# Performance work log

Hardware: AMD Instinct MI355X
Metric: run time of the kernel (lower is better)

Reference implementation:

```python
import jax, jax.numpy as jnp
import numpy as np

# Jamba mamba mixer dims
H = 4096      # hidden_size
D = 8192      # intermediate_size = mamba_expand * hidden_size
N = 16        # ssm_state_size (mamba_d_state)
K = 4         # conv_kernel_size (mamba_d_conv)
R = 256       # time_step_rank (mamba_dt_rank)
BATCH = 1
L = 2048
EPS = 1e-6


def setup_inputs() -> dict:
    key = jax.random.key(0)
    ks = jax.random.split(key, 10)
    s = 0.02
    return {
        "hidden_states": jax.random.normal(ks[0], (BATCH, L, H), jnp.float32),
        "W_in": jax.random.normal(ks[1], (2 * D, H), jnp.float32) * s,
        "conv_w": jax.random.normal(ks[2], (D, K), jnp.float32) * s,
        "conv_b": jax.random.normal(ks[3], (D,), jnp.float32) * s,
        "Wx": jax.random.normal(ks[4], (R + 2 * N, D), jnp.float32) * s,
        "dt_ln_w": jnp.ones((R,), jnp.float32),
        "b_ln_w": jnp.ones((N,), jnp.float32),
        "c_ln_w": jnp.ones((N,), jnp.float32),
        "Wdt": jax.random.normal(ks[5], (D, R), jnp.float32) * s,
        "dt_bias": jax.random.normal(ks[6], (D,), jnp.float32) * s,
        "A": -jnp.exp(jax.random.normal(ks[7], (D, N), jnp.float32) * 0.5),  # A = -exp(A_log)
        "D_param": jnp.ones((D,), jnp.float32),
        "W_out": jax.random.normal(ks[8], (H, D), jnp.float32) * s,
    }


def _rmsnorm(x, w):
    return x * jax.lax.rsqrt(jnp.mean(x * x, axis=-1, keepdims=True) + EPS) * w


def reference(hidden_states, W_in, conv_w, conv_b, Wx, dt_ln_w, b_ln_w, c_ln_w,
              Wdt, dt_bias, A, D_param, W_out):
    # in_proj -> [B, L, 2D]; split into ssm branch and gate
    proj = hidden_states @ W_in.T
    u, gate = jnp.split(proj, 2, axis=-1)

    # causal depthwise conv1d over sequence dim, then SiLU (causal_conv1d_fn)
    x = jnp.transpose(u, (0, 2, 1))  # [B, D, L]
    x = jax.lax.conv_general_dilated(
        x, conv_w[:, None, :], window_strides=(1,), padding=[(K - 1, 0)],
        dimension_numbers=("NCH", "OIH", "NCH"), feature_group_count=D)
    u = jax.nn.silu(jnp.transpose(x, (0, 2, 1)) + conv_b)  # [B, L, D]

    # x_proj -> dt / B / C with RMSNorms
    ssm_p = u @ Wx.T  # [B, L, R + 2N]
    dt, Bm, Cm = jnp.split(ssm_p, [R, R + N], axis=-1)
    dt = _rmsnorm(dt, dt_ln_w)
    Bm = _rmsnorm(Bm, b_ln_w)
    Cm = _rmsnorm(Cm, c_ln_w)

    # dt_proj (skip_bias_add: bias folded into softplus, delta_softplus=True)
    delta = jax.nn.softplus(dt @ Wdt.T + dt_bias)  # [B, L, D]

    # selective scan: state [B, D, N], recurrence over L
    def step(state, xs):
        d_t, B_t, C_t, u_t = xs  # [B,D], [B,N], [B,N], [B,D]
        dA = jnp.exp(d_t[..., None] * A)                       # [B, D, N]
        state = dA * state + (d_t * u_t)[..., None] * B_t[:, None, :]
        y_t = jnp.einsum("bdn,bn->bd", state, C_t)
        return state, y_t

    init = jnp.zeros((hidden_states.shape[0], D, N), hidden_states.dtype)
    xs = (jnp.swapaxes(delta, 0, 1), jnp.swapaxes(Bm, 0, 1),
          jnp.swapaxes(Cm, 0, 1), jnp.swapaxes(u, 0, 1))
    _, ys = jax.lax.scan(step, init, xs)  # ys: [L, B, D]

    y = jnp.swapaxes(ys, 0, 1) + u * D_param   # skip connection u * D
    y = y * jax.nn.silu(gate)                  # gated output
    return y @ W_out.T                         # out_proj -> [B, L, H]
```

## Files before the change

### kernel.cpp

```cpp
#include <hip/hip_runtime.h>
#include <stdint.h>


#define LSEQ 2048
#define HDIM 4096
#define DDIM 8192
#define NST  16
#define NPAD 384
#define NC   16
#define CLEN 128

typedef __bf16 bf16x8 __attribute__((ext_vector_type(8)));
typedef float  f32x4  __attribute__((ext_vector_type(4)));

__device__ __forceinline__ ushort f2b(float f) {
  uint32_t x = __float_as_uint(f);
  x += 0x7FFFu + ((x >> 16) & 1u);
  return (ushort)(x >> 16);
}
__device__ __forceinline__ float b2f(ushort u) {
  return __uint_as_float(((uint32_t)u) << 16);
}

__device__ __forceinline__ void gload_lds16(const ushort* g, ushort* l) {
  __builtin_amdgcn_global_load_lds(
      (const __attribute__((address_space(1))) void*)g,
      (__attribute__((address_space(3))) void*)l, 16, 0, 0);
}

__global__ __launch_bounds__(256) void cvt_kernel(const float* __restrict__ s,
                                                  ushort* __restrict__ d,
                                                  size_t n8) {
  size_t i = (size_t)blockIdx.x * 256 + threadIdx.x;
  if (i >= n8) return;
  const float4* sp = (const float4*)s;
  float4 a = sp[2 * i], b = sp[2 * i + 1];
  union { ushort us[8]; uint4 v; } u;
  u.us[0] = f2b(a.x); u.us[1] = f2b(a.y); u.us[2] = f2b(a.z); u.us[3] = f2b(a.w);
  u.us[4] = f2b(b.x); u.us[5] = f2b(b.y); u.us[6] = f2b(b.z); u.us[7] = f2b(b.w);
  ((uint4*)d)[i] = u.v;
}

template <int MODE, int OUT>
__global__ __launch_bounds__(512, 2) void gemm8p(
    const ushort* __restrict__ A, const ushort* __restrict__ Bw,
    void* __restrict__ Cv, int M, int N, int ldk, int Kc) {
  __shared__ __align__(16) ushort As[2][256 * 64];
  __shared__ __align__(16) ushort Bs[2][256 * 64];
  const int tid  = threadIdx.x;
  const int lane = tid & 63;
  const int w    = tid >> 6;
  const int wr   = w >> 2;
  const int wc   = w & 3;

  const int glob = (blockIdx.z * gridDim.y + blockIdx.y) * gridDim.x + blockIdx.x;
  const int k8 = glob & 7, j = glob >> 3;
  int mt, nt, zz;
  if (MODE == 0) {
    mt = j & 7;
    nt = k8 * (gridDim.x >> 3) + (j >> 3);
    zz = 0;
  } else {
    mt = (k8 & 1) * 4 + (j & 3);
    nt = (k8 >> 1) * 4 + ((j >> 2) & 3);
    zz = j >> 4;
  }
  const int m0 = mt * 256, n0 = nt * 256;
  const int kbeg = zz * Kc;
  const int NT = Kc >> 6;

  const int srck = (lane & 7) ^ ((lane >> 3) & 7);
  const int astripe = w >> 2, awl = w & 3;
  const int arow_st = astripe * 128 + awl * 8 + (lane >> 3);
  const ushort* Abase = A + (size_t)(m0 + arow_st) * ldk + kbeg + srck * 8;
  const int aldsb = (astripe * 128 + awl * 8) * 64;
  const int brow_st = w * 8 + (lane >> 3);
  const ushort* Bbase = Bw + (size_t)(n0 + brow_st) * ldk + kbeg + srck * 8;
  const int bldsb = (w * 8) * 64;

  const int lrow = lane & 15;
  const int kch  = lane >> 4;
  const int axor = lrow & 7;

  auto stA = [&](int buf, int kt, int q) {
    gload_lds16(Abase + (size_t)q * 32 * ldk + kt * 64,
                &As[buf][aldsb + q * 32 * 64]);
  };
  auto stB = [&](int buf, int kt, int half, int jj) {
    gload_lds16(Bbase + (size_t)(half * 128 + jj * 64) * ldk + kt * 64,
                &Bs[buf][bldsb + (half * 128 + jj * 64) * 64]);
  };
  auto rdA = [&](int buf, int mi, int sl) -> bf16x8 {
    int arow = wr * 128 + mi * 16 + lrow;
    int s4 = sl * 4 + kch;
    return *(const bf16x8*)&As[buf][arow * 64 + ((s4 ^ axor) << 3)];
  };
  auto rdB = [&](int buf, int ni, int sl) -> bf16x8 {
    int brow = wc * 64 + ni * 16 + lrow;
    int s4 = sl * 4 + kch;
    return *(const bf16x8*)&Bs[buf][brow * 64 + ((s4 ^ axor) << 3)];
  };

  f32x4 acc[8][4] = {};
  bf16x8 afr[2][2][2];
  bf16x8 bfr[2][4][2];

#define RDAQ(BUF, Q, AP)                                                      \
  { _Pragma("unroll") for (int m2 = 0; m2 < 2; ++m2)                          \
      _Pragma("unroll") for (int sl = 0; sl < 2; ++sl)                        \
        afr[AP][m2][sl] = rdA(BUF, (Q) * 2 + m2, sl); }
#define RDBALL(BUF, BP)                                                       \
  { _Pragma("unroll") for (int ni = 0; ni < 4; ++ni)                          \
      _Pragma("unroll") for (int sl = 0; sl < 2; ++sl)                        \
        bfr[BP][ni][sl] = rdB(BUF, ni, sl); }
#define MFMA16(MQ, AP, BP)                                                    \
  { asm volatile("s_barrier" ::: "memory");                                   \
    __builtin_amdgcn_s_setprio(1);                                            \
    _Pragma("unroll") for (int sl = 0; sl < 2; ++sl)                          \
      _Pragma("unroll") for (int m2 = 0; m2 < 2; ++m2)                        \
        _Pragma("unroll") for (int ni = 0; ni < 4; ++ni)                      \
          acc[(MQ) * 2 + m2][ni] = __builtin_amdgcn_mfma_f32_16x16x32_bf16(   \
              afr[AP][m2][sl], bfr[BP][ni][sl], acc[(MQ) * 2 + m2][ni],       \
              0, 0, 0);                                                       \
    __builtin_amdgcn_s_setprio(0); }

  stB(0, 0, 0, 0); stB(0, 0, 0, 1); stB(0, 0, 1, 0); stB(0, 0, 1, 1);
  stA(0, 0, 0); stA(0, 0, 1); stA(0, 0, 2); stA(0, 0, 3);
  stB(1, 1, 0, 0); stB(1, 1, 0, 1); stB(1, 1, 1, 0); stB(1, 1, 1, 1);
  stA(1, 1, 0); stA(1, 1, 1); stA(1, 1, 2); stA(1, 1, 3);
  asm volatile("s_waitcnt vmcnt(8)" ::: "memory");
  asm volatile("s_barrier" ::: "memory");
  RDBALL(0, 0);
  RDAQ(0, 0, 1);

  for (int t = 0; t < NT; t += 2) {
    const int t2 = (t + 2 < NT) ? t + 2 : 0;
    const int t3 = (t + 3 < NT) ? t + 3 : 0;
    RDAQ(0, 1, 0);
    stB(0, t2, 0, 0); stB(0, t2, 0, 1);
    MFMA16(0, 1, 0);
    RDAQ(0, 2, 1);
    stB(0, t2, 1, 0); stB(0, t2, 1, 1);
    MFMA16(1, 0, 0);
    RDAQ(0, 3, 0);
    stA(0, t2, 0); stA(0, t2, 1);
    MFMA16(2, 1, 0);
    asm volatile("s_waitcnt vmcnt(6)" ::: "memory");
    RDBALL(1, 1);
    RDAQ(1, 0, 1);
    stA(0, t2, 2); stA(0, t2, 3);
    MFMA16(3, 0, 0);
    RDAQ(1, 1, 0);
    stB(1, t3, 0, 0); stB(1, t3, 0, 1);
    MFMA16(0, 1, 1);
    RDAQ(1, 2, 1);
    stB(1, t3, 1, 0); stB(1, t3, 1, 1);
    MFMA16(1, 0, 1);
    RDAQ(1, 3, 0);
    stA(1, t3, 0); stA(1, t3, 1);
    MFMA16(2, 1, 1);
    asm volatile("s_waitcnt vmcnt(6)" ::: "memory");
    RDBALL(0, 0);
    RDAQ(0, 0, 1);
    stA(1, t3, 2); stA(1, t3, 3);
    MFMA16(3, 0, 1);
  }
#undef RDAQ
#undef RDBALL
#undef MFMA16

  asm volatile("s_waitcnt vmcnt(0)" ::: "memory");
  float*  C  = (float*) Cv + (size_t)zz * M * N;
  ushort* Cb = (ushort*)Cv + (size_t)zz * M * N;
#pragma unroll
  for (int mi = 0; mi < 8; ++mi) {
    int row0 = m0 + wr * 128 + mi * 16 + kch * 4;
#pragma unroll
    for (int ni = 0; ni < 4; ++ni) {
      int col = n0 + wc * 64 + ni * 16 + lrow;
#pragma unroll
      for (int q_ = 0; q_ < 4; ++q_) {
        if (OUT == 0)
          C[(size_t)(row0 + q_) * N + col] = acc[mi][ni][q_];
        else
          Cb[(size_t)(row0 + q_) * N + col] = f2b(acc[mi][ni][q_]);
      }
    }
  }
}

template <int EPI, int OBF>
__global__ __launch_bounds__(256) void gemm_nt(
    const ushort* __restrict__ A, const ushort* __restrict__ Bw,
    void* __restrict__ Cv, int M, int N, int ldk, int Kc,
    const float* __restrict__ bias) {
  __shared__ __align__(16) ushort As[128 * 64];
  __shared__ __align__(16) ushort Bs[128 * 64];
  const int tid  = threadIdx.x;
  const int lane = tid & 63;
  const int wid  = tid >> 6;
  const int wr = wid >> 1, wc = wid & 1;
  const int m0 = blockIdx.y * 128, n0 = blockIdx.x * 128;
  const int kbeg = blockIdx.z * Kc;
  float*  C  = (float*) Cv + (size_t)blockIdx.z * M * N;
  ushort* Cb = (ushort*)Cv + (size_t)blockIdx.z * M * N;
  const int rr0 = tid >> 3;
  const int sl  = tid & 7;
  const int lrow = lane & 15;
  const int lks  = lane >> 4;

  f32x4 acc[4][4] = {};

  for (int k0 = kbeg; k0 < kbeg + Kc; k0 += 64) {
#pragma unroll
    for (int i = 0; i < 4; ++i) {
      int rr  = i * 32 + rr0;
      int ksl = sl ^ (rr & 7);
      const ushort* ga = A  + (size_t)(m0 + rr) * ldk + k0 + ksl * 8;
      const ushort* gb = Bw + (size_t)(n0 + rr) * ldk + k0 + ksl * 8;
      ushort* la = As + (i * 256 + (wid << 6)) * 8;
      ushort* lb = Bs + (i * 256 + (wid << 6)) * 8;
      gload_lds16(ga, la);
      gload_lds16(gb, lb);
    }
    __syncthreads();
#pragma unroll
    for (int kc = 0; kc < 2; ++kc) {
      bf16x8 av[4], bv[4];
#pragma unroll
      for (int mi = 0; mi < 4; ++mi) {
        int row = wr * 64 + mi * 16 + lrow;
        int ks  = kc * 4 + lks;
        av[mi] = *(const bf16x8*)(As + row * 64 + ((ks ^ (row & 7)) << 3));
      }
#pragma unroll
      for (int ni = 0; ni < 4; ++ni) {
        int row = wc * 64 + ni * 16 + lrow;
        int ks  = kc * 4 + lks;
        bv[ni] = *(const bf16x8*)(Bs + row * 64 + ((ks ^ (row & 7)) << 3));
      }
#pragma unroll
      for (int mi = 0; mi < 4; ++mi)
#pragma unroll
        for (int ni = 0; ni < 4; ++ni)
          acc[mi][ni] = __builtin_amdgcn_mfma_f32_16x16x32_bf16(
              av[mi], bv[ni], acc[mi][ni], 0, 0, 0);
    }
    __syncthreads();
  }

#pragma unroll
  for (int mi = 0; mi < 4; ++mi) {
    int row0 = m0 + wr * 64 + mi * 16 + (lks << 2);
#pragma unroll
    for (int ni = 0; ni < 4; ++ni) {
      int col = n0 + wc * 64 + ni * 16 + lrow;
      float bcol = 0.f;
      if (EPI == 1) bcol = bias[col];
#pragma unroll
      for (int q = 0; q < 4; ++q) {
        float v = acc[mi][ni][q];
        if (EPI == 1) {
          v += bcol;
          v = (v > 20.f) ? v : log1pf(__expf(v));
        }
        if (OBF == 0) C [(size_t)(row0 + q) * N + col] = v;
        else          Cb[(size_t)(row0 + q) * N + col] = f2b(v);
      }
    }
  }
}

__global__ __launch_bounds__(256) void reduce2_kernel(
    const float* __restrict__ Cp, float* __restrict__ out) {
  size_t i = (size_t)blockIdx.x * 256 + threadIdx.x;
  const size_t MN4 = (size_t)LSEQ * HDIM / 4;
  float4 a = ((const float4*)Cp)[i];
  float4 b = ((const float4*)Cp)[MN4 + i];
  ((float4*)out)[i] = make_float4(a.x + b.x, a.y + b.y, a.z + b.z, a.w + b.w);
}

__global__ __launch_bounds__(256) void conv_silu_kernel(
    const ushort* __restrict__ ub, const float* __restrict__ cw,
    const float* __restrict__ cb, ushort* __restrict__ uc) {
  int d = blockIdx.x * 256 + threadIdx.x;
  int l0 = blockIdx.y * 16;
  float4 w4 = ((const float4*)cw)[d];
  float bsum = cb[d];
  float xm3 = (l0 >= 3) ? b2f(ub[(size_t)(l0 - 3) * DDIM + d]) : 0.f;
  float xm2 = (l0 >= 2) ? b2f(ub[(size_t)(l0 - 2) * DDIM + d]) : 0.f;
  float xm1 = (l0 >= 1) ? b2f(ub[(size_t)(l0 - 1) * DDIM + d]) : 0.f;
#pragma unroll
  for (int i = 0; i < 16; ++i) {
    int l = l0 + i;
    float xc = b2f(ub[(size_t)l * DDIM + d]);
    float s = bsum + w4.x * xm3 + w4.y * xm2 + w4.z * xm1 + w4.w * xc;
    float o = s / (1.f + __expf(-s));
    uc[(size_t)l * DDIM + d] = f2b(o);
    xm3 = xm2; xm2 = xm1; xm1 = xc;
  }
}

__global__ __launch_bounds__(64) void norms_kernel(
    const float* __restrict__ Cp, const float* __restrict__ dtw,
    const float* __restrict__ bw, const float* __restrict__ cwn,
    ushort* __restrict__ dtn, float* __restrict__ Bn, float* __restrict__ Cn) {
  int l = blockIdx.x, lane = threadIdx.x;
  const size_t MN = (size_t)LSEQ * NPAD;
  const float* row = Cp + (size_t)l * NPAD;
  float va[4] = {0.f, 0.f, 0.f, 0.f};
#pragma unroll
  for (int z = 0; z < 8; ++z) {
    float4 v = ((const float4*)(row + z * MN))[lane];
    va[0] += v.x; va[1] += v.y; va[2] += v.z; va[3] += v.w;
  }
  float ss = va[0]*va[0] + va[1]*va[1] + va[2]*va[2] + va[3]*va[3];
#pragma unroll
  for (int m = 32; m >= 1; m >>= 1) ss += __shfl_xor(ss, m);
  float rs = rsqrtf(ss * (1.f / 256.f) + 1e-6f);
  float4 wv = ((const float4*)dtw)[lane];
  float wa[4] = {wv.x, wv.y, wv.z, wv.w};
  union { ushort us[4]; uint2 v2; } o;
#pragma unroll
  for (int jj = 0; jj < 4; ++jj) o.us[jj] = f2b(va[jj] * rs * wa[jj]);
  ((uint2*)(dtn + (size_t)l * 256))[lane] = o.v2;

  int g = lane & 15;
  float bv = 0.f, cv = 0.f;
#pragma unroll
  for (int z = 0; z < 8; ++z) {
    bv += row[z * MN + 256 + g];
    cv += row[z * MN + 272 + g];
  }
  float bs = bv * bv, cs = cv * cv;
#pragma unroll
  for (int m = 8; m >= 1; m >>= 1) {
    bs += __shfl_xor(bs, m);
    cs += __shfl_xor(cs, m);
  }
  if (lane < 16) {
    Bn[(size_t)l * NST + lane] = bv * rsqrtf(bs * (1.f / 16.f) + 1e-6f) * bw[lane];
    Cn[(size_t)l * NST + lane] = cv * rsqrtf(cs * (1.f / 16.f) + 1e-6f) * cwn[lane];
  }
}

__global__ __launch_bounds__(256) void scan_phase1(
    const ushort* __restrict__ delta, const ushort* __restrict__ uc,
    const float* __restrict__ Bn, const float* __restrict__ Am,
    float* __restrict__ Sbuf, float* __restrict__ Pbuf) {
  __shared__ float sB[CLEN * NST];
  const int tid = threadIdx.x;
  const int d = blockIdx.x * 256 + tid;
  const int c = blockIdx.y, l0 = c * CLEN;
  {
    const float4* bsrc = (const float4*)(Bn + (size_t)l0 * NST);
    float4* bdst = (float4*)sB;
    for (int i = tid; i < CLEN * NST / 4; i += 256) bdst[i] = bsrc[i];
  }
  __syncthreads();
  float A[16];
#pragma unroll
  for (int jj = 0; jj < 4; ++jj) {
    float4 a4 = ((const float4*)(Am + (size_t)d * NST))[jj];
    A[4*jj] = a4.x; A[4*jj+1] = a4.y; A[4*jj+2] = a4.z; A[4*jj+3] = a4.w;
  }
  float st[16] = {};
  float sd = 0.f;
  const size_t base = (size_t)l0 * DDIM + d;
  float dx0 = b2f(delta[base]),  dx1 = b2f(delta[base + DDIM]);
  float ux0 = b2f(uc[base]),     ux1 = b2f(uc[base + DDIM]);
  for (int l = 0; l < CLEN; l += 2) {
    int lp = (l + 2 < CLEN) ? l + 2 : CLEN - 2;
    float dxn0 = b2f(delta[base + (size_t)lp * DDIM]);
    float dxn1 = b2f(delta[base + (size_t)(lp + 1) * DDIM]);
    float uxn0 = b2f(uc[base + (size_t)lp * DDIM]);
    float uxn1 = b2f(uc[base + (size_t)(lp + 1) * DDIM]);
    sd += dx0;
    float dxu = dx0 * ux0;
#pragma unroll
    for (int n = 0; n < 16; ++n)
      st[n] = fmaf(__expf(dx0 * A[n]), st[n], dxu * sB[l * NST + n]);
    sd += dx1;
    dxu = dx1 * ux1;
#pragma unroll
    for (int n = 0; n < 16; ++n)
      st[n] = fmaf(__expf(dx1 * A[n]), st[n], dxu * sB[(l + 1) * NST + n]);
    dx0 = dxn0; dx1 = dxn1; ux0 = uxn0; ux1 = uxn1;
  }
  float4* Sd = (float4*)(Sbuf + ((size_t)c * DDIM + d) * NST);
  float4* Pd = (float4*)(Pbuf + ((size_t)c * DDIM + d) * NST);
#pragma unroll
  for (int jj = 0; jj < 4; ++jj) {
    Sd[jj] = make_float4(st[4*jj], st[4*jj+1], st[4*jj+2], st[4*jj+3]);
    Pd[jj] = make_float4(__expf(A[4*jj] * sd),   __expf(A[4*jj+1] * sd),
                         __expf(A[4*jj+2] * sd), __expf(A[4*jj+3] * sd));
  }
}

__global__ __launch_bounds__(256) void scan_phase2(
    const float* __restrict__ Sbuf, float* __restrict__ Pbuf) {
  size_t t = (size_t)blockIdx.x * 256 + threadIdx.x;
  const size_t stride = (size_t)DDIM * NST;
  float s = 0.f;
  for (int c = 0; c < NC; ++c) {
    float P = Pbuf[c * stride + t];
    float S = Sbuf[c * stride + t];
    Pbuf[c * stride + t] = s;
    s = fmaf(P, s, S);
  }
}

__global__ __launch_bounds__(256) void scan_phase3(
    const ushort* __restrict__ delta, const ushort* __restrict__ uc,
    const float* __restrict__ Bn, const float* __restrict__ Cn,
    const float* __restrict__ Am, const float* __restrict__ Ibuf,
    const ushort* __restrict__ gbuf, const float* __restrict__ Dp,
    ushort* __restrict__ yg) {
  __shared__ float sB[CLEN * NST];
  __shared__ float sC[CLEN * NST];
  const int tid = threadIdx.x;
  const int d = blockIdx.x * 256 + tid;
  const int c = blockIdx.y, l0 = c * CLEN;
  {
    const float4* bsrc = (const float4*)(Bn + (size_t)l0 * NST);
    const float4* csrc = (const float4*)(Cn + (size_t)l0 * NST);
    float4* bdst = (float4*)sB;
    float4* cdst = (float4*)sC;
    for (int i = tid; i < CLEN * NST / 4; i += 256) {
      bdst[i] = bsrc[i];
      cdst[i] = csrc[i];
    }
  }
  __syncthreads();
  float A[16], st[16];
#pragma unroll
  for (int jj = 0; jj < 4; ++jj) {
    float4 a4 = ((const float4*)(Am + (size_t)d * NST))[jj];
    A[4*jj] = a4.x; A[4*jj+1] = a4.y; A[4*jj+2] = a4.z; A[4*jj+3] = a4.w;
    float4 s4 = ((const float4*)(Ibuf + ((size_t)c * DDIM + d) * NST))[jj];
    st[4*jj] = s4.x; st[4*jj+1] = s4.y; st[4*jj+2] = s4.z; st[4*jj+3] = s4.w;
  }
  const float Dpd = Dp[d];
  const size_t base = (size_t)l0 * DDIM + d;
  float dx0 = b2f(delta[base]),   dx1 = b2f(delta[base + DDIM]);
  float ux0 = b2f(uc[base]),      ux1 = b2f(uc[base + DDIM]);
  float g0  = b2f(gbuf[base]),    g1  = b2f(gbuf[base + DDIM]);
  for (int l = 0; l < CLEN; l += 2) {
    int lp = (l + 2 < CLEN) ? l + 2 : CLEN - 2;
    float dxn0 = b2f(delta[base + (size_t)lp * DDIM]);
    float dxn1 = b2f(delta[base + (size_t)(lp + 1) * DDIM]);
    float uxn0 = b2f(uc[base + (size_t)lp * DDIM]);
    float uxn1 = b2f(uc[base + (size_t)(lp + 1) * DDIM]);
    float gn0  = b2f(gbuf[base + (size_t)lp * DDIM]);
    float gn1  = b2f(gbuf[base + (size_t)(lp + 1) * DDIM]);
    {
      float dxu = dx0 * ux0, y0 = 0.f, y1 = 0.f;
#pragma unroll
      for (int n = 0; n < 16; n += 2) {
        st[n]   = fmaf(__expf(dx0 * A[n]),   st[n],   dxu * sB[l * NST + n]);
        st[n+1] = fmaf(__expf(dx0 * A[n+1]), st[n+1], dxu * sB[l * NST + n+1]);
        y0 = fmaf(st[n],   sC[l * NST + n],   y0);
        y1 = fmaf(st[n+1], sC[l * NST + n+1], y1);
      }
      float o = (y0 + y1 + ux0 * Dpd) * (g0 / (1.f + __expf(-g0)));
      yg[base + (size_t)l * DDIM] = f2b(o);
    }
    {
      float dxu = dx1 * ux1, y0 = 0.f, y1 = 0.f;
#pragma unroll
      for (int n = 0; n < 16; n += 2) {
        st[n]   = fmaf(__expf(dx1 * A[n]),   st[n],   dxu * sB[(l+1) * NST + n]);
        st[n+1] = fmaf(__expf(dx1 * A[n+1]), st[n+1], dxu * sB[(l+1) * NST + n+1]);
        y0 = fmaf(st[n],   sC[(l+1) * NST + n],   y0);
        y1 = fmaf(st[n+1], sC[(l+1) * NST + n+1], y1);
      }
      float o = (y0 + y1 + ux1 * Dpd) * (g1 / (1.f + __expf(-g1)));
      yg[base + (size_t)(l + 1) * DDIM] = f2b(o);
    }
    dx0 = dxn0; dx1 = dxn1; ux0 = uxn0; ux1 = uxn1; g0 = gn0; g1 = gn1;
  }
}

extern "C" void kernel_launch(void* const* d_in, const int* in_sizes, int n_in,
                              void* d_out, int out_size, void* d_ws, size_t ws_size,
                              hipStream_t stream) {
  (void)in_sizes; (void)n_in; (void)out_size; (void)ws_size;
  const float* hs   = (const float*)d_in[0];
  const float* W_in = (const float*)d_in[1];
  const float* cw   = (const float*)d_in[2];
  const float* cb   = (const float*)d_in[3];
  const float* Wx   = (const float*)d_in[4];
  const float* dtw  = (const float*)d_in[5];
  const float* bw   = (const float*)d_in[6];
  const float* cwn  = (const float*)d_in[7];
  const float* Wdt  = (const float*)d_in[8];
  const float* dtb  = (const float*)d_in[9];
  const float* Am   = (const float*)d_in[10];
  const float* Dp   = (const float*)d_in[11];
  const float* Wout = (const float*)d_in[12];
  float* out = (float*)d_out;

  char* ws = (char*)d_ws;
  const size_t MB = 1ull << 20;
  ushort* win_b   = (ushort*)(ws);
  ushort* delta_b = (ushort*)(ws);
  ushort* wout_b  = (ushort*)(ws + 64 * MB);
  ushort* ubuf   = (ushort*)(ws + 128 * MB);
  float*  Cp     = (float*) (ws + 128 * MB);
  float*  Cp2    = (float*) (ws + 128 * MB);
  float*  Sbuf   = (float*) (ws + 152 * MB);
  float*  Pbuf   = (float*) (ws + 160 * MB);
  ushort* gbuf   = (ushort*)(ws + 192 * MB);
  ushort* hs_b   = (ushort*)(ws + 256 * MB);
  ushort* wxp_b  = (ushort*)(ws + 272 * MB);
  ushort* wdt_b  = (ushort*)(ws + 278 * MB);
  ushort* ucv    = (ushort*)(ws + 282 * MB);
  ushort* dtn    = (ushort*)(ws + 317 * MB);
  float*  Bn     = (float*) (ws + 318 * MB);
  float*  Cn     = (float*) (ws + 318 * MB + 131072);
  ushort* yg     = (ushort*)(ws + 319 * MB);

  cvt_kernel<<<67108864 / 2048, 256, 0, stream>>>(W_in, win_b, 67108864 / 8);
  cvt_kernel<<<8388608 / 2048, 256, 0, stream>>>(hs, hs_b, 8388608 / 8);
  cvt_kernel<<<2359296 / 2048, 256, 0, stream>>>(Wx, wxp_b, 2359296 / 8);
  hipMemsetAsync((char*)wxp_b + 4718592, 0, 1572864, stream);
  cvt_kernel<<<2097152 / 2048, 256, 0, stream>>>(Wdt, wdt_b, 2097152 / 8);

  gemm8p<0, 1><<<dim3(32, 8), 512, 0, stream>>>(hs_b, win_b, ubuf,
                                                2048, DDIM, 4096, 4096);
  gemm8p<0, 1><<<dim3(32, 8), 512, 0, stream>>>(hs_b, win_b + (size_t)DDIM * 4096,
                                                gbuf, 2048, DDIM, 4096, 4096);
  cvt_kernel<<<33554432 / 2048, 256, 0, stream>>>(Wout, wout_b, 33554432 / 8);

  conv_silu_kernel<<<dim3(32, 128), 256, 0, stream>>>(ubuf, cw, cb, ucv);

  gemm_nt<0, 0><<<dim3(3, 16, 8), 256, 0, stream>>>(ucv, wxp_b, Cp,
                                                    2048, NPAD, 8192, 1024,
                                                    nullptr);
  norms_kernel<<<2048, 64, 0, stream>>>(Cp, dtw, bw, cwn, dtn, Bn, Cn);

  gemm_nt<1, 1><<<dim3(64, 16), 256, 0, stream>>>(dtn, wdt_b, delta_b,
                                                  2048, DDIM, 256, 256, dtb);

  scan_phase1<<<dim3(32, NC), 256, 0, stream>>>(delta_b, ucv, Bn, Am, Sbuf, Pbuf);
  scan_phase2<<<512, 256, 0, stream>>>(Sbuf, Pbuf);
  scan_phase3<<<dim3(32, NC), 256, 0, stream>>>(delta_b, ucv, Bn, Cn, Am, Pbuf,
                                                gbuf, Dp, yg);

  gemm8p<1, 0><<<dim3(16, 8, 2), 512, 0, stream>>>(yg, wout_b, Cp2,
                                                   2048, HDIM, 8192, 4096);
  reduce2_kernel<<<(LSEQ * HDIM / 4) / 256, 256, 0, stream>>>(Cp2, out);
}
```

Baseline: 813.3 us.

## Merge in_proj GEMMs into one launch and re-schedule gemm8p main loop

The two in_proj GEMMs (u and gate halves) become a single gemm8p launch of 64x8 tiles writing an interleaved [L, 2D] buffer, and the conv and scan kernels read u and gate from it with a 16384-element row stride. The gemm8p main loop is reordered: A-tile stores for the next stage are moved earlier and s_barrier instructions are inserted between MFMA groups to keep waves in lockstep. The split-K tile mapping for the out_proj mode is also changed so the K-halves are interleaved differently. This is meant to remove a launch and tail effect and to improve load/compute overlap, at the cost of more barriers and a wider-strided gate/u buffer, which may hurt cache locality.

```diff
diff --git a/kernel.cpp b/kernel.cpp
--- a/kernel.cpp
+++ b/kernel.cpp
@@ -9,6 +9,7 @@
 #define NPAD 384
 #define NC   16
 #define CLEN 128
+#define PGLD 16384
 
 typedef __bf16 bf16x8 __attribute__((ext_vector_type(8)));
 typedef float  f32x4  __attribute__((ext_vector_type(4)));
@@ -61,9 +62,9 @@
     nt = k8 * (gridDim.x >> 3) + (j >> 3);
     zz = 0;
   } else {
-    mt = (k8 & 1) * 4 + (j & 3);
-    nt = (k8 >> 1) * 4 + ((j >> 2) & 3);
-    zz = j >> 4;
+    mt = j & 7;
+    nt = (k8 >> 1) * 4 + (j >> 3);
+    zz = k8 & 1;
   }
   const int m0 = mt * 256, n0 = nt * 256;
   const int kbeg = zz * Kc;
@@ -137,33 +138,43 @@
     const int t2 = (t + 2 < NT) ? t + 2 : 0;
     const int t3 = (t + 3 < NT) ? t + 3 : 0;
     RDAQ(0, 1, 0);
+    stA(1, t + 1, 2); stA(1, t + 1, 3);
+    MFMA16(0, 1, 0);
+    asm volatile("s_barrier" ::: "memory");
+    RDAQ(0, 2, 1);
     stB(0, t2, 0, 0); stB(0, t2, 0, 1);
-    MFMA16(0, 1, 0);
-    RDAQ(0, 2, 1);
+    MFMA16(1, 0, 0);
+    asm volatile("s_barrier" ::: "memory");
+    RDAQ(0, 3, 0);
     stB(0, t2, 1, 0); stB(0, t2, 1, 1);
-    MFMA16(1, 0, 0);
-    RDAQ(0, 3, 0);
+    MFMA16(2, 1, 0);
+    asm volatile("s_barrier" ::: "memory");
     stA(0, t2, 0); stA(0, t2, 1);
-    MFMA16(2, 1, 0);
     asm volatile("s_waitcnt vmcnt(6)" ::: "memory");
+    asm volatile("s_barrier" ::: "memory");
     RDBALL(1, 1);
     RDAQ(1, 0, 1);
+    MFMA16(3, 0, 0);
+    asm volatile("s_barrier" ::: "memory");
+    RDAQ(1, 1, 0);
     stA(0, t2, 2); stA(0, t2, 3);
-    MFMA16(3, 0, 0);
-    RDAQ(1, 1, 0);
+    MFMA16(0, 1, 1);
+    asm volatile("s_barrier" ::: "memory");
+    RDAQ(1, 2, 1);
     stB(1, t3, 0, 0); stB(1, t3, 0, 1);
-    MFMA16(0, 1, 1);
-    RDAQ(1, 2, 1);
+    MFMA16(1, 0, 1);
+    asm volatile("s_barrier" ::: "memory");
+    RDAQ(1, 3, 0);
     stB(1, t3, 1, 0); stB(1, t3, 1, 1);
-    MFMA16(1, 0, 1);
-    RDAQ(1, 3, 0);
+    MFMA16(2, 1, 1);
+    asm volatile("s_barrier" ::: "memory");
     stA(1, t3, 0); stA(1, t3, 1);
-    MFMA16(2, 1, 1);
     asm volatile("s_waitcnt vmcnt(6)" ::: "memory");
+    asm volatile("s_barrier" ::: "memory");
     RDBALL(0, 0);
     RDAQ(0, 0, 1);
-    stA(1, t3, 2); stA(1, t3, 3);
     MFMA16(3, 0, 1);
+    asm volatile("s_barrier" ::: "memory");
   }
 #undef RDAQ
 #undef RDBALL
@@ -281,19 +292,19 @@
 }
 
 __global__ __launch_bounds__(256) void conv_silu_kernel(
-    const ushort* __restrict__ ub, const float* __restrict__ cw,
+    const ushort* __restrict__ pg, const float* __restrict__ cw,
     const float* __restrict__ cb, ushort* __restrict__ uc) {
   int d = blockIdx.x * 256 + threadIdx.x;
   int l0 = blockIdx.y * 16;
   float4 w4 = ((const float4*)cw)[d];
   float bsum = cb[d];
-  float xm3 = (l0 >= 3) ? b2f(ub[(size_t)(l0 - 3) * DDIM + d]) : 0.f;
-  float xm2 = (l0 >= 2) ? b2f(ub[(size_t)(l0 - 2) * DDIM + d]) : 0.f;
-  float xm1 = (l0 >= 1) ? b2f(ub[(size_t)(l0 - 1) * DDIM + d]) : 0.f;
+  float xm3 = (l0 >= 3) ? b2f(pg[(size_t)(l0 - 3) * PGLD + d]) : 0.f;
+  float xm2 = (l0 >= 2) ? b2f(pg[(size_t)(l0 - 2) * PGLD + d]) : 0.f;
+  float xm1 = (l0 >= 1) ? b2f(pg[(size_t)(l0 - 1) * PGLD + d]) : 0.f;
 #pragma unroll
   for (int i = 0; i < 16; ++i) {
     int l = l0 + i;
-    float xc = b2f(ub[(size_t)l * DDIM + d]);
+    float xc = b2f(pg[(size_t)l * PGLD + d]);
     float s = bsum + w4.x * xm3 + w4.y * xm2 + w4.z * xm1 + w4.w * xc;
     float o = s / (1.f + __expf(-s));
     uc[(size_t)l * DDIM + d] = f2b(o);
@@ -414,7 +425,7 @@
     const ushort* __restrict__ delta, const ushort* __restrict__ uc,
     const float* __restrict__ Bn, const float* __restrict__ Cn,
     const float* __restrict__ Am, const float* __restrict__ Ibuf,
-    const ushort* __restrict__ gbuf, const float* __restrict__ Dp,
+    const ushort* __restrict__ gb, const float* __restrict__ Dp,
     ushort* __restrict__ yg) {
   __shared__ float sB[CLEN * NST];
   __shared__ float sC[CLEN * NST];
@@ -441,18 +452,19 @@
     st[4*jj] = s4.x; st[4*jj+1] = s4.y; st[4*jj+2] = s4.z; st[4*jj+3] = s4.w;
   }
   const float Dpd = Dp[d];
-  const size_t base = (size_t)l0 * DDIM + d;
+  const size_t base  = (size_t)l0 * DDIM + d;
+  const size_t base2 = (size_t)l0 * PGLD + d;
   float dx0 = b2f(delta[base]),   dx1 = b2f(delta[base + DDIM]);
   float ux0 = b2f(uc[base]),      ux1 = b2f(uc[base + DDIM]);
-  float g0  = b2f(gbuf[base]),    g1  = b2f(gbuf[base + DDIM]);
+  float g0  = b2f(gb[base2]),     g1  = b2f(gb[base2 + PGLD]);
   for (int l = 0; l < CLEN; l += 2) {
     int lp = (l + 2 < CLEN) ? l + 2 : CLEN - 2;
     float dxn0 = b2f(delta[base + (size_t)lp * DDIM]);
     float dxn1 = b2f(delta[base + (size_t)(lp + 1) * DDIM]);
     float uxn0 = b2f(uc[base + (size_t)lp * DDIM]);
     float uxn1 = b2f(uc[base + (size_t)(lp + 1) * DDIM]);
-    float gn0  = b2f(gbuf[base + (size_t)lp * DDIM]);
-    float gn1  = b2f(gbuf[base + (size_t)(lp + 1) * DDIM]);
+    float gn0  = b2f(gb[base2 + (size_t)lp * PGLD]);
+    float gn1  = b2f(gb[base2 + (size_t)(lp + 1) * PGLD]);
     {
       float dxu = dx0 * ux0, y0 = 0.f, y1 = 0.f;
 #pragma unroll
@@ -505,12 +517,11 @@
   ushort* win_b   = (ushort*)(ws);
   ushort* delta_b = (ushort*)(ws);
   ushort* wout_b  = (ushort*)(ws + 64 * MB);
-  ushort* ubuf   = (ushort*)(ws + 128 * MB);
-  float*  Cp     = (float*) (ws + 128 * MB);
+  ushort* pg     = (ushort*)(ws + 128 * MB);
   float*  Cp2    = (float*) (ws + 128 * MB);
-  float*  Sbuf   = (float*) (ws + 152 * MB);
-  float*  Pbuf   = (float*) (ws + 160 * MB);
-  ushort* gbuf   = (ushort*)(ws + 192 * MB);
+  float*  Cp     = (float*) (ws + 192 * MB);
+  float*  Sbuf   = (float*) (ws + 216 * MB);
+  float*  Pbuf   = (float*) (ws + 224 * MB);
   ushort* hs_b   = (ushort*)(ws + 256 * MB);
   ushort* wxp_b  = (ushort*)(ws + 272 * MB);
   ushort* wdt_b  = (ushort*)(ws + 278 * MB);
@@ -526,13 +537,11 @@
   hipMemsetAsync((char*)wxp_b + 4718592, 0, 1572864, stream);
   cvt_kernel<<<2097152 / 2048, 256, 0, stream>>>(Wdt, wdt_b, 2097152 / 8);
 
-  gemm8p<0, 1><<<dim3(32, 8), 512, 0, stream>>>(hs_b, win_b, ubuf,
-                                                2048, DDIM, 4096, 4096);
-  gemm8p<0, 1><<<dim3(32, 8), 512, 0, stream>>>(hs_b, win_b + (size_t)DDIM * 4096,
-                                                gbuf, 2048, DDIM, 4096, 4096);
+  gemm8p<0, 1><<<dim3(64, 8), 512, 0, stream>>>(hs_b, win_b, pg,
+                                                2048, PGLD, 4096, 4096);
   cvt_kernel<<<33554432 / 2048, 256, 0, stream>>>(Wout, wout_b, 33554432 / 8);
 
-  conv_silu_kernel<<<dim3(32, 128), 256, 0, stream>>>(ubuf, cw, cb, ucv);
+  conv_silu_kernel<<<dim3(32, 128), 256, 0, stream>>>(pg, cw, cb, ucv);
 
   gemm_nt<0, 0><<<dim3(3, 16, 8), 256, 0, stream>>>(ucv, wxp_b, Cp,
                                                     2048, NPAD, 8192, 1024,
@@ -545,7 +554,7 @@
   scan_phase1<<<dim3(32, NC), 256, 0, stream>>>(delta_b, ucv, Bn, Am, Sbuf, Pbuf);
   scan_phase2<<<512, 256, 0, stream>>>(Sbuf, Pbuf);
   scan_phase3<<<dim3(32, NC), 256, 0, stream>>>(delta_b, ucv, Bn, Cn, Am, Pbuf,
-                                                gbuf, Dp, yg);
+                                                pg + DDIM, Dp, yg);
 
   gemm8p<1, 0><<<dim3(16, 8, 2), 512, 0, stream>>>(yg, wout_b, Cp2,
                                                    2048, HDIM, 8192, 4096);
```

Measured after the change: 906.6 us. 1.11x slower.

## Restructure GEMM main loop to single-buffered fragments with explicit barriers and remap split-K tiles

Applied to the files above, without the earlier changes.

The GEMM inner loop drops double-buffered register fragments (afr/bfr ping-pong) in favour of single fragment sets, adding an lgkmcnt(0) wait, a sched_barrier and a trailing s_barrier around each MFMA group. The prologue now issues only half of the second A tile, and the remainder is loaded at the start of each iteration. The MODE 1 block-to-tile mapping changes so that the split-K index comes from k8 rather than j. The aim is lower register pressure and different L2 locality, at the cost of more barriers and less overlap between LDS reads and MFMA.

```diff
diff --git a/kernel.cpp b/kernel.cpp
--- a/kernel.cpp
+++ b/kernel.cpp
@@ -61,9 +61,9 @@
     nt = k8 * (gridDim.x >> 3) + (j >> 3);
     zz = 0;
   } else {
-    mt = (k8 & 1) * 4 + (j & 3);
-    nt = (k8 >> 1) * 4 + ((j >> 2) & 3);
-    zz = j >> 4;
+    mt = j & 7;
+    nt = (k8 >> 1) * 4 + (j >> 3);
+    zz = k8 & 1;
   }
   const int m0 = mt * 256, n0 = nt * 256;
   const int kbeg = zz * Kc;
@@ -102,72 +102,70 @@
   };
 
   f32x4 acc[8][4] = {};
-  bf16x8 afr[2][2][2];
-  bf16x8 bfr[2][4][2];
-
-#define RDAQ(BUF, Q, AP)                                                      \
+  bf16x8 afr[2][2];
+  bf16x8 bfr[4][2];
+
+#define RDAQ(BUF, Q)                                                          \
   { _Pragma("unroll") for (int m2 = 0; m2 < 2; ++m2)                          \
       _Pragma("unroll") for (int sl = 0; sl < 2; ++sl)                        \
-        afr[AP][m2][sl] = rdA(BUF, (Q) * 2 + m2, sl); }
-#define RDBALL(BUF, BP)                                                       \
+        afr[m2][sl] = rdA(BUF, (Q) * 2 + m2, sl); }
+#define RDBALL(BUF)                                                           \
   { _Pragma("unroll") for (int ni = 0; ni < 4; ++ni)                          \
       _Pragma("unroll") for (int sl = 0; sl < 2; ++sl)                        \
-        bfr[BP][ni][sl] = rdB(BUF, ni, sl); }
-#define MFMA16(MQ, AP, BP)                                                    \
+        bfr[ni][sl] = rdB(BUF, ni, sl); }
+#define SYNC_MFMA(MQ)                                                         \
   { asm volatile("s_barrier" ::: "memory");                                   \
+    asm volatile("s_waitcnt lgkmcnt(0)" ::: "memory");                        \
+    __builtin_amdgcn_sched_barrier(0);                                        \
     __builtin_amdgcn_s_setprio(1);                                            \
     _Pragma("unroll") for (int sl = 0; sl < 2; ++sl)                          \
       _Pragma("unroll") for (int m2 = 0; m2 < 2; ++m2)                        \
         _Pragma("unroll") for (int ni = 0; ni < 4; ++ni)                      \
           acc[(MQ) * 2 + m2][ni] = __builtin_amdgcn_mfma_f32_16x16x32_bf16(   \
-              afr[AP][m2][sl], bfr[BP][ni][sl], acc[(MQ) * 2 + m2][ni],       \
-              0, 0, 0);                                                       \
-    __builtin_amdgcn_s_setprio(0); }
+              afr[m2][sl], bfr[ni][sl], acc[(MQ) * 2 + m2][ni], 0, 0, 0);     \
+    __builtin_amdgcn_s_setprio(0);                                            \
+    asm volatile("s_barrier" ::: "memory"); }
 
   stB(0, 0, 0, 0); stB(0, 0, 0, 1); stB(0, 0, 1, 0); stB(0, 0, 1, 1);
   stA(0, 0, 0); stA(0, 0, 1); stA(0, 0, 2); stA(0, 0, 3);
   stB(1, 1, 0, 0); stB(1, 1, 0, 1); stB(1, 1, 1, 0); stB(1, 1, 1, 1);
-  stA(1, 1, 0); stA(1, 1, 1); stA(1, 1, 2); stA(1, 1, 3);
-  asm volatile("s_waitcnt vmcnt(8)" ::: "memory");
+  stA(1, 1, 0); stA(1, 1, 1);
+  asm volatile("s_waitcnt vmcnt(6)" ::: "memory");
   asm volatile("s_barrier" ::: "memory");
-  RDBALL(0, 0);
-  RDAQ(0, 0, 1);
 
   for (int t = 0; t < NT; t += 2) {
     const int t2 = (t + 2 < NT) ? t + 2 : 0;
     const int t3 = (t + 3 < NT) ? t + 3 : 0;
-    RDAQ(0, 1, 0);
+    RDBALL(0); RDAQ(0, 0);
+    stA(1, t + 1, 2); stA(1, t + 1, 3);
+    SYNC_MFMA(0);
+    RDAQ(0, 1);
     stB(0, t2, 0, 0); stB(0, t2, 0, 1);
-    MFMA16(0, 1, 0);
-    RDAQ(0, 2, 1);
+    SYNC_MFMA(1);
+    RDAQ(0, 2);
     stB(0, t2, 1, 0); stB(0, t2, 1, 1);
-    MFMA16(1, 0, 0);
-    RDAQ(0, 3, 0);
+    SYNC_MFMA(2);
+    RDAQ(0, 3);
     stA(0, t2, 0); stA(0, t2, 1);
-    MFMA16(2, 1, 0);
     asm volatile("s_waitcnt vmcnt(6)" ::: "memory");
-    RDBALL(1, 1);
-    RDAQ(1, 0, 1);
+    SYNC_MFMA(3);
+    RDBALL(1); RDAQ(1, 0);
     stA(0, t2, 2); stA(0, t2, 3);
-    MFMA16(3, 0, 0);
-    RDAQ(1, 1, 0);
+    SYNC_MFMA(0);
+    RDAQ(1, 1);
     stB(1, t3, 0, 0); stB(1, t3, 0, 1);
-    MFMA16(0, 1, 1);
-    RDAQ(1, 2, 1);
+    SYNC_MFMA(1);
+    RDAQ(1, 2);
     stB(1, t3, 1, 0); stB(1, t3, 1, 1);
-    MFMA16(1, 0, 1);
-    RDAQ(1, 3, 0);
+    SYNC_MFMA(2);
+    RDAQ(1, 3);
     stA(1, t3, 0); stA(1, t3, 1);
-    MFMA16(2, 1, 1);
     asm volatile("s_waitcnt vmcnt(6)" ::: "memory");
-    RDBALL(0, 0);
-    RDAQ(0, 0, 1);
-    stA(1, t3, 2); stA(1, t3, 3);
-    MFMA16(3, 0, 1);
+    SYNC_MFMA(3);
   }
 #undef RDAQ
 #undef RDBALL
-#undef MFMA16
+#undef SYNC_MFMA
 
   asm volatile("s_waitcnt vmcnt(0)" ::: "memory");
   float*  C  = (float*) Cv + (size_t)zz * M * N;
@@ -414,7 +412,7 @@
     const ushort* __restrict__ delta, const ushort* __restrict__ uc,
     const float* __restrict__ Bn, const float* __restrict__ Cn,
     const float* __restrict__ Am, const float* __restrict__ Ibuf,
-    const ushort* __restrict__ gbuf, const float* __restrict__ Dp,
+    const ushort* __restrict__ gb, const float* __restrict__ Dp,
     ushort* __restrict__ yg) {
   __shared__ float sB[CLEN * NST];
   __shared__ float sC[CLEN * NST];
@@ -444,15 +442,15 @@
   const size_t base = (size_t)l0 * DDIM + d;
   float dx0 = b2f(delta[base]),   dx1 = b2f(delta[base + DDIM]);
   float ux0 = b2f(uc[base]),      ux1 = b2f(uc[base + DDIM]);
-  float g0  = b2f(gbuf[base]),    g1  = b2f(gbuf[base + DDIM]);
+  float g0  = b2f(gb[base]),      g1  = b2f(gb[base + DDIM]);
   for (int l = 0; l < CLEN; l += 2) {
     int lp = (l + 2 < CLEN) ? l + 2 : CLEN - 2;
     float dxn0 = b2f(delta[base + (size_t)lp * DDIM]);
     float dxn1 = b2f(delta[base + (size_t)(lp + 1) * DDIM]);
     float uxn0 = b2f(uc[base + (size_t)lp * DDIM]);
     float uxn1 = b2f(uc[base + (size_t)(lp + 1) * DDIM]);
-    float gn0  = b2f(gbuf[base + (size_t)lp * DDIM]);
-    float gn1  = b2f(gbuf[base + (size_t)(lp + 1) * DDIM]);
+    float gn0  = b2f(gb[base + (size_t)lp * DDIM]);
+    float gn1  = b2f(gb[base + (size_t)(lp + 1) * DDIM]);
     {
       float dxu = dx0 * ux0, y0 = 0.f, y1 = 0.f;
 #pragma unroll
```

Result: slower. 839.3 us (+3.2%).
